# Performance work log

Measured on AMD Instinct MI355X. Metric: run time of the kernel, lower is better.

Reference implementation:

```python
import jax, jax.numpy as jnp
import numpy as np

B, V, NFEAT, INTER, NHID1, NHID12, NCLASS = 131072, 8, 32, 8, 16, 8, 2


def setup_inputs() -> dict:
    key = jax.random.key(0)
    ks = jax.random.split(key, 16)
    # node feature tensor: channel 0 = node type in {0,1}, channels 1..32 = features
    types = jax.random.randint(ks[0], (B, V, 1), 0, 2).astype(jnp.float32)
    feats = jax.random.normal(ks[1], (B, V, NFEAT), dtype=jnp.float32)
    x = jnp.concatenate([types, feats], axis=-1)  # (B, V, 33)
    adj = jax.random.uniform(ks[2], (B, V, V), dtype=jnp.float32)
    edge_attr = jax.random.normal(ks[3], (B, V, V), dtype=jnp.float32)
    s = lambda k, *sh: jax.random.normal(k, sh, dtype=jnp.float32) * 0.1
    return {
        "x": x, "adj": adj, "edge_attr": edge_attr,
        "wa": s(ks[4], INTER, NFEAT), "ba": jnp.zeros((INTER,), jnp.float32),
        "wb": s(ks[5], INTER, NFEAT), "bb": jnp.zeros((INTER,), jnp.float32),
        "w1": s(ks[6], NFEAT, NHID1), "b1": jnp.zeros((NHID1,), jnp.float32),
        "w2": s(ks[7], NHID1, NHID12), "b2": jnp.zeros((NHID12,), jnp.float32),
        "wg": s(ks[8], NHID12, NHID12), "bg": jnp.zeros((NHID12,), jnp.float32),
        "wf": s(ks[9], NCLASS, NHID12), "bf": jnp.zeros((NCLASS,), jnp.float32),
    }


def _attn_pool(h, wg, bg):
    # GlobalAttentionPooling: softmax(gate_nn(h)) over nodes, weighted sum
    gate = jax.nn.softmax(jnp.einsum('bvc,oc->bvo', h, wg) + bg, axis=1)
    return jnp.sum(gate * h, axis=1)  # (B, NHID12)


def reference(x, adj, edge_attr, wa, ba, wb, bb, w1, b1, w2, b2, wg, bg, wf, bf):
    node_types = x[..., 0]           # (B, V)
    feat = x[..., 1:]                # (B, V, 32)
    # conv_b (1x1 conv == per-node linear), output layout (B, inter, V)
    Fk = jnp.einsum('bvc,oc->bov', feat, wb) + bb[None, :, None]  # (B, 8, V=8)
    S = jax.nn.softmax(jnp.matmul(Fk, Fk), axis=1)                # (B, 8, 8)
    W = adj * (S + edge_attr)                                     # (B, V, V)
    # graph conv 1: (W @ feat) @ w1 + b1, LeakyReLU(0.01)
    h = jax.nn.leaky_relu(jnp.einsum('bvw,bwc->bvc', W, feat) @ w1 + b1)
    # graph conv 2
    h = jax.nn.leaky_relu(jnp.einsum('bvw,bwc->bvc', W, h) @ w2 + b2)  # (B, V, 8)
    # per-type masked attention pooling; types fixed to {0, 1}
    pooled = []
    for t in (0.0, 1.0):
        mask = (node_types == t)[..., None].astype(h.dtype)
        pooled.append(_attn_pool(h * mask, wg, bg))
    x_pool = jnp.mean(jnp.stack(pooled, axis=1), axis=1)  # (B, NHID12)
    return x_pool @ wf.T + bf  # (B, NCLASS)
```

## Files before the change

### kernel.cpp

```cpp
#include <hip/hip_runtime.h>


#define SLOTS 32
#define NTHREADS 256

typedef float v2f __attribute__((ext_vector_type(2)));
typedef float4 __attribute__((aligned(4))) f4u;

__device__ __forceinline__ float grp_sum8(float x) {
    x += __shfl_xor(x, 1);
    x += __shfl_xor(x, 2);
    x += __shfl_xor(x, 4);
    return x;
}
__device__ __forceinline__ void wavefence() { __builtin_amdgcn_wave_barrier(); }
__device__ __forceinline__ v2f mkv(float a, float b) { v2f r; r.x = a; r.y = b; return r; }


#define KSTEP(kk, cb) { \
    const float4 qk = *(const float4*)(SB + v * 16 + ((((kk) + (v >> 1) + sl) & 3) << 2)); \
    const v2f fA = mkv(qk.x, qk.y), fB = mkv(qk.z, qk.w); \
    _Pragma("unroll") \
    for (int o = 0; o < 8; ++o) { \
        Fko[o] = __builtin_elementwise_fma(fA, *(const v2f*)(wb + o * 32 + (cb)),     Fko[o]); \
        Fko[o] = __builtin_elementwise_fma(fB, *(const v2f*)(wb + o * 32 + (cb) + 2), Fko[o]); \
    } \
    const float fu[4] = { qk.x, qk.y, qk.z, qk.w }; \
    _Pragma("unroll") \
    for (int u = 0; u < 4; ++u) { \
        const int c = (cb) + u; \
        const v2f f2 = mkv(fu[u], fu[u]); \
        _Pragma("unroll") \
        for (int p = 0; p < 8; ++p) \
            g12[p] = __builtin_elementwise_fma(f2, *(const v2f*)(w1 + c * 16 + 2 * p), g12[p]); \
    } }

__global__ __launch_bounds__(NTHREADS, 4)
void gcn_fused(const float* __restrict__ x,
               const float* __restrict__ adj,
               const float* __restrict__ edge,
               const float* __restrict__ wb, const float* __restrict__ bb,
               const float* __restrict__ w1, const float* __restrict__ b1,
               const float* __restrict__ w2, const float* __restrict__ b2,
               const float* __restrict__ wg,
               const float* __restrict__ wf, const float* __restrict__ bf,
               float* __restrict__ out, int nGroups)
{
    __shared__ __align__(16) float lds[4480];

    const int tid  = threadIdx.x;
    const int slot = tid >> 3;
    const int v    = tid & 7;
    const int sl   = slot & 7;
    float* SB = &lds[(slot >> 3) * 1120 + sl * 140];
    float* A  = SB + 64;

    long long bb_ = (long long)blockIdx.x * SLOTS + slot;
    if (bb_ >= (long long)nGroups * SLOTS) bb_ = (long long)nGroups * SLOTS - 1;
    const size_t b = (size_t)bb_;

    const float* xb = x + b * 264;
    const int nb = v & 4;
    const int cl = v & 3;
    float4 xa[4];
#pragma unroll
    for (int i = 0; i < 4; ++i)
        xa[i] = *(const f4u*)(xb + (nb + i) * 33 + 1 + cl * 4);

    const float4* ar = (const float4*)(adj  + b * 64 + (size_t)v * 8);
    const float4* er = (const float4*)(edge + b * 64 + (size_t)v * 8);
    const float4 a0 = ar[0], a1 = ar[1];
    const float4 e0 = er[0], e1 = er[1];
    const float type = xb[v * 33];

#pragma unroll
    for (int i = 0; i < 4; ++i) {
        const int n = nb + i;
        *(float4*)(SB + n * 16 + (((cl + (n >> 1) + sl) & 3) << 2)) = xa[i];
    }
    float4 xc[4];
#pragma unroll
    for (int i = 0; i < 4; ++i)
        xc[i] = *(const f4u*)(xb + (nb + i) * 33 + 17 + cl * 4);
    wavefence();

    v2f Fko[8];
#pragma unroll
    for (int o = 0; o < 8; ++o) Fko[o] = mkv(0.f, 0.f);
    v2f g12[8];
#pragma unroll
    for (int p = 0; p < 8; ++p) g12[p] = mkv(0.f, 0.f);

    KSTEP(0, 0) KSTEP(1, 4) KSTEP(2, 8) KSTEP(3, 12)
    wavefence();
#pragma unroll
    for (int i = 0; i < 4; ++i) {
        const int n = nb + i;
        *(float4*)(SB + n * 16 + (((cl + (n >> 1) + sl) & 3) << 2)) = xc[i];
    }
    wavefence();
    KSTEP(0, 16) KSTEP(1, 20) KSTEP(2, 24) KSTEP(3, 28)
    wavefence();

    float Fks[8];
#pragma unroll
    for (int o = 0; o < 8; ++o) Fks[o] = Fko[o].x + Fko[o].y + bb[o];

#pragma unroll
    for (int o = 0; o < 8; ++o) A[o * 8 + v] = Fks[o];
    {
        float4* gp = (float4*)(SB + v * 8);
        gp[0] = make_float4(g12[0].x, g12[0].y, g12[1].x, g12[1].y);
        gp[1] = make_float4(g12[2].x, g12[2].y, g12[3].x, g12[3].y);
    }
    wavefence();

    v2f Fk2[4];
#pragma unroll
    for (int p = 0; p < 4; ++p) Fk2[p] = mkv(Fks[2 * p], Fks[2 * p + 1]);

    float M[8];
#pragma unroll
    for (int o = 0; o < 8; ++o) {
        const float4* fr = (const float4*)(A + o * 8);
        const float4 r0 = fr[0], r1 = fr[1];
        v2f acc = mkv(0.f, 0.f);
        acc = __builtin_elementwise_fma(mkv(r0.x, r0.y), Fk2[0], acc);
        acc = __builtin_elementwise_fma(mkv(r0.z, r0.w), Fk2[1], acc);
        acc = __builtin_elementwise_fma(mkv(r1.x, r1.y), Fk2[2], acc);
        acc = __builtin_elementwise_fma(mkv(r1.z, r1.w), Fk2[3], acc);
        M[o] = acc.x + acc.y;
    }
    wavefence();
    float mx = M[0];
#pragma unroll
    for (int o = 1; o < 8; ++o) mx = fmaxf(mx, M[o]);
    float ssum = 0.f;
#pragma unroll
    for (int o = 0; o < 8; ++o) { M[o] = __expf(M[o] - mx); ssum += M[o]; }
    const float sinv = 1.f / ssum;
#pragma unroll
    for (int o = 0; o < 8; ++o) A[o * 8 + v] = M[o] * sinv;
    wavefence();

    const float4* sr = (const float4*)(A + v * 8);
    const float4 s0 = sr[0], s1 = sr[1];
    v2f W2[4];
    W2[0] = mkv(a0.x, a0.y) * (mkv(s0.x, s0.y) + mkv(e0.x, e0.y));
    W2[1] = mkv(a0.z, a0.w) * (mkv(s0.z, s0.w) + mkv(e0.z, e0.w));
    W2[2] = mkv(a1.x, a1.y) * (mkv(s1.x, s1.y) + mkv(e1.x, e1.y));
    W2[3] = mkv(a1.z, a1.w) * (mkv(s1.z, s1.w) + mkv(e1.z, e1.w));

    v2f m1[8];
#pragma unroll
    for (int p = 0; p < 8; ++p) m1[p] = mkv(0.f, 0.f);
#pragma unroll
    for (int w = 0; w < 8; ++w) {
        const float wv = (w & 1) ? W2[w >> 1].y : W2[w >> 1].x;
        const v2f f2 = mkv(wv, wv);
        const float4* gp = (const float4*)(SB + w * 8);
        const float4 q0 = gp[0], q1 = gp[1];
        m1[0] = __builtin_elementwise_fma(f2, mkv(q0.x, q0.y), m1[0]);
        m1[1] = __builtin_elementwise_fma(f2, mkv(q0.z, q0.w), m1[1]);
        m1[2] = __builtin_elementwise_fma(f2, mkv(q1.x, q1.y), m1[2]);
        m1[3] = __builtin_elementwise_fma(f2, mkv(q1.z, q1.w), m1[3]);
    }
    wavefence();
    {
        float4* gp = (float4*)(SB + v * 8);
        gp[0] = make_float4(g12[4].x, g12[4].y, g12[5].x, g12[5].y);
        gp[1] = make_float4(g12[6].x, g12[6].y, g12[7].x, g12[7].y);
    }
    wavefence();
#pragma unroll
    for (int w = 0; w < 8; ++w) {
        const float wv = (w & 1) ? W2[w >> 1].y : W2[w >> 1].x;
        const v2f f2 = mkv(wv, wv);
        const float4* gp = (const float4*)(SB + w * 8);
        const float4 q0 = gp[0], q1 = gp[1];
        m1[4] = __builtin_elementwise_fma(f2, mkv(q0.x, q0.y), m1[4]);
        m1[5] = __builtin_elementwise_fma(f2, mkv(q0.z, q0.w), m1[5]);
        m1[6] = __builtin_elementwise_fma(f2, mkv(q1.x, q1.y), m1[6]);
        m1[7] = __builtin_elementwise_fma(f2, mkv(q1.z, q1.w), m1[7]);
    }
    v2f h[8];
    {
        const v2f k01 = mkv(0.01f, 0.01f);
#pragma unroll
        for (int p = 0; p < 8; ++p) {
            const v2f t = m1[p] + *(const v2f*)(b1 + 2 * p);
            h[p] = __builtin_elementwise_max(t, t * k01);
        }
    }

    v2f g22[4];
#pragma unroll
    for (int p = 0; p < 4; ++p) g22[p] = mkv(0.f, 0.f);
#pragma unroll
    for (int j = 0; j < 16; ++j) {
        const float hv = (j & 1) ? h[j >> 1].y : h[j >> 1].x;
        const v2f f2 = mkv(hv, hv);
#pragma unroll
        for (int p = 0; p < 4; ++p)
            g22[p] = __builtin_elementwise_fma(f2, *(const v2f*)(w2 + j * 8 + 2 * p), g22[p]);
    }
    wavefence();
    {
        float4* gp = (float4*)(SB + v * 8);
        gp[0] = make_float4(g22[0].x, g22[0].y, g22[1].x, g22[1].y);
        gp[1] = make_float4(g22[2].x, g22[2].y, g22[3].x, g22[3].y);
    }
    wavefence();

    v2f m2[4];
#pragma unroll
    for (int p = 0; p < 4; ++p) m2[p] = mkv(0.f, 0.f);
#pragma unroll
    for (int w = 0; w < 8; ++w) {
        const float wv = (w & 1) ? W2[w >> 1].y : W2[w >> 1].x;
        const v2f f2 = mkv(wv, wv);
        const float4* gp = (const float4*)(SB + w * 8);
        const float4 q0 = gp[0], q1 = gp[1];
        m2[0] = __builtin_elementwise_fma(f2, mkv(q0.x, q0.y), m2[0]);
        m2[1] = __builtin_elementwise_fma(f2, mkv(q0.z, q0.w), m2[1]);
        m2[2] = __builtin_elementwise_fma(f2, mkv(q1.x, q1.y), m2[2]);
        m2[3] = __builtin_elementwise_fma(f2, mkv(q1.z, q1.w), m2[3]);
    }
    v2f h2[4];
    {
        const v2f k01 = mkv(0.01f, 0.01f);
#pragma unroll
        for (int p = 0; p < 4; ++p) {
            const v2f t = m2[p] + *(const v2f*)(b2 + 2 * p);
            h2[p] = __builtin_elementwise_max(t, t * k01);
        }
    }

    float Ys[8];
#pragma unroll
    for (int o = 0; o < 8; ++o) {
        v2f acc = mkv(0.f, 0.f);
#pragma unroll
        for (int p = 0; p < 4; ++p)
            acc = __builtin_elementwise_fma(h2[p], *(const v2f*)(wg + o * 8 + 2 * p), acc);
        Ys[o] = acc.x + acc.y;
    }
    wavefence();
    {
        float4* pp = (float4*)(SB + v * 16);
        pp[0] = make_float4(Ys[0], h2[0].x, Ys[1], h2[0].y);
        pp[1] = make_float4(Ys[2], h2[1].x, Ys[3], h2[1].y);
        pp[2] = make_float4(Ys[4], h2[2].x, Ys[5], h2[2].y);
        pp[3] = make_float4(Ys[6], h2[3].x, Ys[7], h2[3].y);
        SB[128 + v] = type;
    }
    wavefence();

    const int o = v;
    float yc[8], hc[8], ty[8];
#pragma unroll
    for (int vp = 0; vp < 8; ++vp) {
        const float2 q = *(const float2*)(SB + vp * 16 + o * 2);
        yc[vp] = q.x;
        hc[vp] = q.y;
        ty[vp] = SB[128 + vp];
    }
    float xp = 0.f;
#pragma unroll
    for (int t = 0; t < 2; ++t) {
        const float tv = (float)t;
        float l[8];
        float lmx = -1e30f;
#pragma unroll
        for (int vp = 0; vp < 8; ++vp) {
            l[vp] = (ty[vp] == tv) ? yc[vp] : 0.f;
            lmx = fmaxf(lmx, l[vp]);
        }
        float esum = 0.f, num = 0.f;
#pragma unroll
        for (int vp = 0; vp < 8; ++vp) {
            const float e = __expf(l[vp] - lmx);
            esum += e;
            num  += (ty[vp] == tv) ? e * hc[vp] : 0.f;
        }
        xp += 0.5f * num / esum;
    }

    const float y0 = grp_sum8(xp * wf[0 * 8 + o]);
    const float y1 = grp_sum8(xp * wf[1 * 8 + o]);
    if (v == 0) {
        float2* op = (float2*)(out + b * 2);
        *op = make_float2(y0 + bf[0], y1 + bf[1]);
    }
}

extern "C" void kernel_launch(void* const* d_in, const int* in_sizes, int n_in,
                              void* d_out, int out_size, void* d_ws, size_t ws_size,
                              hipStream_t stream) {
    const float* x    = (const float*)d_in[0];
    const float* adj  = (const float*)d_in[1];
    const float* edge = (const float*)d_in[2];
    const float* wb   = (const float*)d_in[5];
    const float* bb   = (const float*)d_in[6];
    const float* w1   = (const float*)d_in[7];
    const float* b1   = (const float*)d_in[8];
    const float* w2   = (const float*)d_in[9];
    const float* b2   = (const float*)d_in[10];
    const float* wg   = (const float*)d_in[11];
    const float* wf   = (const float*)d_in[13];
    const float* bf   = (const float*)d_in[14];
    float* out = (float*)d_out;

    const int Btot    = in_sizes[0] / 264;
    const int nGroups = (Btot + SLOTS - 1) / SLOTS;

    gcn_fused<<<nGroups, NTHREADS, 0, stream>>>(x, adj, edge, wb, bb, w1, b1,
                                                w2, b2, wg, wf, bf, out, nGroups);
}
```

Before: 273.2 us.

## Process two graphs per thread group to reuse weight loads and raise ILP

Each 8-thread group now handles two graphs instead of one (64 graphs per block), sharing each weight load across both graphs in the conv, graph-conv and pooling stages. LDS per block doubles, and the adj/edge loads are moved later to overlap with the first feature pass. The aim is to amortise scalar and constant weight loads and expose more independent FMAs per thread. The cost is higher register and LDS pressure, which may reduce occupancy under the 4-blocks launch bound.

New measurement: 283.4 us. 1.04x slower.

```diff
diff --git a/kernel.cpp b/kernel.cpp
--- a/kernel.cpp
+++ b/kernel.cpp
@@ -1,7 +1,7 @@
 #include <hip/hip_runtime.h>
 
 
-#define SLOTS 32
+#define SLOTS 64
 #define NTHREADS 256
 
 typedef float v2f __attribute__((ext_vector_type(2)));
@@ -15,24 +15,37 @@
 }
 __device__ __forceinline__ void wavefence() { __builtin_amdgcn_wave_barrier(); }
 __device__ __forceinline__ v2f mkv(float a, float b) { v2f r; r.x = a; r.y = b; return r; }
-
-
-#define KSTEP(kk, cb) { \
-    const float4 qk = *(const float4*)(SB + v * 16 + ((((kk) + (v >> 1) + sl) & 3) << 2)); \
-    const v2f fA = mkv(qk.x, qk.y), fB = mkv(qk.z, qk.w); \
+__device__ __forceinline__ v2f vfma(v2f a, v2f b, v2f c) { return __builtin_elementwise_fma(a, b, c); }
+
+
+#define KSTEP2(kk, cb) { \
+    const int cell = (((kk) + (v >> 1) + sl) & 3) << 2; \
+    const float4 qA = *(const float4*)(SB0 + v * 16 + cell); \
+    const float4 qB = *(const float4*)(SB1 + v * 16 + cell); \
+    const v2f fA01 = mkv(qA.x, qA.y), fA23 = mkv(qA.z, qA.w); \
+    const v2f fB01 = mkv(qB.x, qB.y), fB23 = mkv(qB.z, qB.w); \
     _Pragma("unroll") \
     for (int o = 0; o < 8; ++o) { \
-        Fko[o] = __builtin_elementwise_fma(fA, *(const v2f*)(wb + o * 32 + (cb)),     Fko[o]); \
-        Fko[o] = __builtin_elementwise_fma(fB, *(const v2f*)(wb + o * 32 + (cb) + 2), Fko[o]); \
+        const v2f w01 = *(const v2f*)(wb + o * 32 + (cb)); \
+        const v2f w23 = *(const v2f*)(wb + o * 32 + (cb) + 2); \
+        Fko[0][o] = vfma(fA01, w01, Fko[0][o]); \
+        Fko[0][o] = vfma(fA23, w23, Fko[0][o]); \
+        Fko[1][o] = vfma(fB01, w01, Fko[1][o]); \
+        Fko[1][o] = vfma(fB23, w23, Fko[1][o]); \
     } \
-    const float fu[4] = { qk.x, qk.y, qk.z, qk.w }; \
+    const float fuA[4] = { qA.x, qA.y, qA.z, qA.w }; \
+    const float fuB[4] = { qB.x, qB.y, qB.z, qB.w }; \
     _Pragma("unroll") \
     for (int u = 0; u < 4; ++u) { \
         const int c = (cb) + u; \
-        const v2f f2 = mkv(fu[u], fu[u]); \
+        const v2f fa = mkv(fuA[u], fuA[u]); \
+        const v2f fb = mkv(fuB[u], fuB[u]); \
         _Pragma("unroll") \
-        for (int p = 0; p < 8; ++p) \
-            g12[p] = __builtin_elementwise_fma(f2, *(const v2f*)(w1 + c * 16 + 2 * p), g12[p]); \
+        for (int p = 0; p < 8; ++p) { \
+            const v2f wp = *(const v2f*)(w1 + c * 16 + 2 * p); \
+            g12[0][p] = vfma(fa, wp, g12[0][p]); \
+            g12[1][p] = vfma(fb, wp, g12[1][p]); \
+        } \
     } }
 
 __global__ __launch_bounds__(NTHREADS, 4)
@@ -46,251 +59,321 @@
                const float* __restrict__ wf, const float* __restrict__ bf,
                float* __restrict__ out, int nGroups)
 {
-    __shared__ __align__(16) float lds[4480];
+    __shared__ __align__(16) float lds[8960];
 
     const int tid  = threadIdx.x;
     const int slot = tid >> 3;
     const int v    = tid & 7;
     const int sl   = slot & 7;
-    float* SB = &lds[(slot >> 3) * 1120 + sl * 140];
-    float* A  = SB + 64;
-
-    long long bb_ = (long long)blockIdx.x * SLOTS + slot;
-    if (bb_ >= (long long)nGroups * SLOTS) bb_ = (long long)nGroups * SLOTS - 1;
-    const size_t b = (size_t)bb_;
-
-    const float* xb = x + b * 264;
+    float* SB0 = &lds[(tid >> 6) * 2240 + sl * 140];
+    float* SB1 = SB0 + 1120;
+    float* SBg[2] = { SB0, SB1 };
+
+    long long base = (long long)blockIdx.x * SLOTS + slot;
+    const long long bmax = (long long)nGroups * SLOTS - 1;
+    size_t b[2];
+#pragma unroll
+    for (int g = 0; g < 2; ++g) {
+        long long t = base + g * 32;
+        if (t > bmax) t = bmax;
+        b[g] = (size_t)t;
+    }
+
+    const float wfv0 = wf[v], wfv1 = wf[8 + v];
+
+    const float* xb[2] = { x + b[0] * 264, x + b[1] * 264 };
     const int nb = v & 4;
     const int cl = v & 3;
-    float4 xa[4];
-#pragma unroll
-    for (int i = 0; i < 4; ++i)
-        xa[i] = *(const f4u*)(xb + (nb + i) * 33 + 1 + cl * 4);
-
-    const float4* ar = (const float4*)(adj  + b * 64 + (size_t)v * 8);
-    const float4* er = (const float4*)(edge + b * 64 + (size_t)v * 8);
-    const float4 a0 = ar[0], a1 = ar[1];
-    const float4 e0 = er[0], e1 = er[1];
-    const float type = xb[v * 33];
-
-#pragma unroll
-    for (int i = 0; i < 4; ++i) {
-        const int n = nb + i;
-        *(float4*)(SB + n * 16 + (((cl + (n >> 1) + sl) & 3) << 2)) = xa[i];
-    }
-    float4 xc[4];
-#pragma unroll
-    for (int i = 0; i < 4; ++i)
-        xc[i] = *(const f4u*)(xb + (nb + i) * 33 + 17 + cl * 4);
-    wavefence();
-
-    v2f Fko[8];
-#pragma unroll
-    for (int o = 0; o < 8; ++o) Fko[o] = mkv(0.f, 0.f);
-    v2f g12[8];
-#pragma unroll
-    for (int p = 0; p < 8; ++p) g12[p] = mkv(0.f, 0.f);
-
-    KSTEP(0, 0) KSTEP(1, 4) KSTEP(2, 8) KSTEP(3, 12)
-    wavefence();
-#pragma unroll
-    for (int i = 0; i < 4; ++i) {
-        const int n = nb + i;
-        *(float4*)(SB + n * 16 + (((cl + (n >> 1) + sl) & 3) << 2)) = xc[i];
-    }
-    wavefence();
-    KSTEP(0, 16) KSTEP(1, 20) KSTEP(2, 24) KSTEP(3, 28)
-    wavefence();
-
-    float Fks[8];
-#pragma unroll
-    for (int o = 0; o < 8; ++o) Fks[o] = Fko[o].x + Fko[o].y + bb[o];
-
-#pragma unroll
-    for (int o = 0; o < 8; ++o) A[o * 8 + v] = Fks[o];
-    {
-        float4* gp = (float4*)(SB + v * 8);
-        gp[0] = make_float4(g12[0].x, g12[0].y, g12[1].x, g12[1].y);
-        gp[1] = make_float4(g12[2].x, g12[2].y, g12[3].x, g12[3].y);
-    }
-    wavefence();
-
-    v2f Fk2[4];
-#pragma unroll
-    for (int p = 0; p < 4; ++p) Fk2[p] = mkv(Fks[2 * p], Fks[2 * p + 1]);
-
-    float M[8];
-#pragma unroll
-    for (int o = 0; o < 8; ++o) {
-        const float4* fr = (const float4*)(A + o * 8);
-        const float4 r0 = fr[0], r1 = fr[1];
-        v2f acc = mkv(0.f, 0.f);
-        acc = __builtin_elementwise_fma(mkv(r0.x, r0.y), Fk2[0], acc);
-        acc = __builtin_elementwise_fma(mkv(r0.z, r0.w), Fk2[1], acc);
-        acc = __builtin_elementwise_fma(mkv(r1.x, r1.y), Fk2[2], acc);
-        acc = __builtin_elementwise_fma(mkv(r1.z, r1.w), Fk2[3], acc);
-        M[o] = acc.x + acc.y;
-    }
-    wavefence();
-    float mx = M[0];
-#pragma unroll
-    for (int o = 1; o < 8; ++o) mx = fmaxf(mx, M[o]);
-    float ssum = 0.f;
-#pragma unroll
-    for (int o = 0; o < 8; ++o) { M[o] = __expf(M[o] - mx); ssum += M[o]; }
-    const float sinv = 1.f / ssum;
-#pragma unroll
-    for (int o = 0; o < 8; ++o) A[o * 8 + v] = M[o] * sinv;
-    wavefence();
-
-    const float4* sr = (const float4*)(A + v * 8);
-    const float4 s0 = sr[0], s1 = sr[1];
-    v2f W2[4];
-    W2[0] = mkv(a0.x, a0.y) * (mkv(s0.x, s0.y) + mkv(e0.x, e0.y));
-    W2[1] = mkv(a0.z, a0.w) * (mkv(s0.z, s0.w) + mkv(e0.z, e0.w));
-    W2[2] = mkv(a1.x, a1.y) * (mkv(s1.x, s1.y) + mkv(e1.x, e1.y));
-    W2[3] = mkv(a1.z, a1.w) * (mkv(s1.z, s1.w) + mkv(e1.z, e1.w));
-
-    v2f m1[8];
-#pragma unroll
-    for (int p = 0; p < 8; ++p) m1[p] = mkv(0.f, 0.f);
-#pragma unroll
-    for (int w = 0; w < 8; ++w) {
-        const float wv = (w & 1) ? W2[w >> 1].y : W2[w >> 1].x;
-        const v2f f2 = mkv(wv, wv);
-        const float4* gp = (const float4*)(SB + w * 8);
-        const float4 q0 = gp[0], q1 = gp[1];
-        m1[0] = __builtin_elementwise_fma(f2, mkv(q0.x, q0.y), m1[0]);
-        m1[1] = __builtin_elementwise_fma(f2, mkv(q0.z, q0.w), m1[1]);
-        m1[2] = __builtin_elementwise_fma(f2, mkv(q1.x, q1.y), m1[2]);
-        m1[3] = __builtin_elementwise_fma(f2, mkv(q1.z, q1.w), m1[3]);
-    }
-    wavefence();
-    {
-        float4* gp = (float4*)(SB + v * 8);
-        gp[0] = make_float4(g12[4].x, g12[4].y, g12[5].x, g12[5].y);
-        gp[1] = make_float4(g12[6].x, g12[6].y, g12[7].x, g12[7].y);
-    }
-    wavefence();
-#pragma unroll
-    for (int w = 0; w < 8; ++w) {
-        const float wv = (w & 1) ? W2[w >> 1].y : W2[w >> 1].x;
-        const v2f f2 = mkv(wv, wv);
-        const float4* gp = (const float4*)(SB + w * 8);
-        const float4 q0 = gp[0], q1 = gp[1];
-        m1[4] = __builtin_elementwise_fma(f2, mkv(q0.x, q0.y), m1[4]);
-        m1[5] = __builtin_elementwise_fma(f2, mkv(q0.z, q0.w), m1[5]);
-        m1[6] = __builtin_elementwise_fma(f2, mkv(q1.x, q1.y), m1[6]);
-        m1[7] = __builtin_elementwise_fma(f2, mkv(q1.z, q1.w), m1[7]);
-    }
-    v2f h[8];
+    float4 xa[2][4];
+#pragma unroll
+    for (int g = 0; g < 2; ++g)
+#pragma unroll
+        for (int i = 0; i < 4; ++i)
+            xa[g][i] = *(const f4u*)(xb[g] + (nb + i) * 33 + 1 + cl * 4);
+
+#pragma unroll
+    for (int g = 0; g < 2; ++g) SBg[g][128 + v] = xb[g][v * 33];
+
+#pragma unroll
+    for (int g = 0; g < 2; ++g)
+#pragma unroll
+        for (int i = 0; i < 4; ++i) {
+            const int n = nb + i;
+            *(float4*)(SBg[g] + n * 16 + (((cl + (n >> 1) + sl) & 3) << 2)) = xa[g][i];
+        }
+    float4 xc[2][4];
+#pragma unroll
+    for (int g = 0; g < 2; ++g)
+#pragma unroll
+        for (int i = 0; i < 4; ++i)
+            xc[g][i] = *(const f4u*)(xb[g] + (nb + i) * 33 + 17 + cl * 4);
+    wavefence();
+
+    v2f Fko[2][8];
+    v2f g12[2][8];
+#pragma unroll
+    for (int g = 0; g < 2; ++g)
+#pragma unroll
+        for (int p = 0; p < 8; ++p) { Fko[g][p] = mkv(0.f, 0.f); g12[g][p] = mkv(0.f, 0.f); }
+
+    KSTEP2(0, 0) KSTEP2(1, 4) KSTEP2(2, 8) KSTEP2(3, 12)
+    wavefence();
+#pragma unroll
+    for (int g = 0; g < 2; ++g)
+#pragma unroll
+        for (int i = 0; i < 4; ++i) {
+            const int n = nb + i;
+            *(float4*)(SBg[g] + n * 16 + (((cl + (n >> 1) + sl) & 3) << 2)) = xc[g][i];
+        }
+    wavefence();
+
+    float4 a0[2], a1[2], e0[2], e1[2];
+#pragma unroll
+    for (int g = 0; g < 2; ++g) {
+        const float4* ar = (const float4*)(adj  + b[g] * 64 + (size_t)v * 8);
+        const float4* er = (const float4*)(edge + b[g] * 64 + (size_t)v * 8);
+        a0[g] = ar[0]; a1[g] = ar[1];
+        e0[g] = er[0]; e1[g] = er[1];
+    }
+
+    KSTEP2(0, 16) KSTEP2(1, 20) KSTEP2(2, 24) KSTEP2(3, 28)
+    wavefence();
+
+    float Fks[2][8];
+#pragma unroll
+    for (int g = 0; g < 2; ++g)
+#pragma unroll
+        for (int o = 0; o < 8; ++o) Fks[g][o] = Fko[g][o].x + Fko[g][o].y + bb[o];
+
+#pragma unroll
+    for (int g = 0; g < 2; ++g) {
+        float* A = SBg[g] + 64;
+#pragma unroll
+        for (int o = 0; o < 8; ++o) A[o * 8 + v] = Fks[g][o];
+        float4* gp = (float4*)(SBg[g] + v * 8);
+        gp[0] = make_float4(g12[g][0].x, g12[g][0].y, g12[g][1].x, g12[g][1].y);
+        gp[1] = make_float4(g12[g][2].x, g12[g][2].y, g12[g][3].x, g12[g][3].y);
+    }
+    wavefence();
+
+    v2f Fk2[2][4];
+#pragma unroll
+    for (int g = 0; g < 2; ++g)
+#pragma unroll
+        for (int p = 0; p < 4; ++p) Fk2[g][p] = mkv(Fks[g][2 * p], Fks[g][2 * p + 1]);
+
+    float M[2][8];
+#pragma unroll
+    for (int g = 0; g < 2; ++g) {
+        const float* A = SBg[g] + 64;
+#pragma unroll
+        for (int o = 0; o < 8; ++o) {
+            const float4* fr = (const float4*)(A + o * 8);
+            const float4 r0 = fr[0], r1 = fr[1];
+            v2f acc = mkv(0.f, 0.f);
+            acc = vfma(mkv(r0.x, r0.y), Fk2[g][0], acc);
+            acc = vfma(mkv(r0.z, r0.w), Fk2[g][1], acc);
+            acc = vfma(mkv(r1.x, r1.y), Fk2[g][2], acc);
+            acc = vfma(mkv(r1.z, r1.w), Fk2[g][3], acc);
+            M[g][o] = acc.x + acc.y;
+        }
+    }
+    wavefence();
+
+#pragma unroll
+    for (int g = 0; g < 2; ++g) {
+        float mx = M[g][0];
+#pragma unroll
+        for (int o = 1; o < 8; ++o) mx = fmaxf(mx, M[g][o]);
+        float ssum = 0.f;
+#pragma unroll
+        for (int o = 0; o < 8; ++o) { M[g][o] = __expf(M[g][o] - mx); ssum += M[g][o]; }
+        const float sinv = 1.f / ssum;
+        float* A = SBg[g] + 64;
+#pragma unroll
+        for (int o = 0; o < 8; ++o) A[o * 8 + v] = M[g][o] * sinv;
+    }
+    wavefence();
+
+    v2f W2[2][4];
+#pragma unroll
+    for (int g = 0; g < 2; ++g) {
+        const float4* sr = (const float4*)(SBg[g] + 64 + v * 8);
+        const float4 s0 = sr[0], s1 = sr[1];
+        W2[g][0] = mkv(a0[g].x, a0[g].y) * (mkv(s0.x, s0.y) + mkv(e0[g].x, e0[g].y));
+        W2[g][1] = mkv(a0[g].z, a0[g].w) * (mkv(s0.z, s0.w) + mkv(e0[g].z, e0[g].w));
+        W2[g][2] = mkv(a1[g].x, a1[g].y) * (mkv(s1.x, s1.y) + mkv(e1[g].x, e1[g].y));
+        W2[g][3] = mkv(a1[g].z, a1[g].w) * (mkv(s1.z, s1.w) + mkv(e1[g].z, e1[g].w));
+    }
+
+    v2f m1[2][8];
+#pragma unroll
+    for (int g = 0; g < 2; ++g)
+#pragma unroll
+        for (int p = 0; p < 8; ++p) m1[g][p] = mkv(0.f, 0.f);
+#pragma unroll
+    for (int g = 0; g < 2; ++g)
+#pragma unroll
+        for (int w = 0; w < 8; ++w) {
+            const float wv = (w & 1) ? W2[g][w >> 1].y : W2[g][w >> 1].x;
+            const v2f f2 = mkv(wv, wv);
+            const float4* gp = (const float4*)(SBg[g] + w * 8);
+            const float4 q0 = gp[0], q1 = gp[1];
+            m1[g][0] = vfma(f2, mkv(q0.x, q0.y), m1[g][0]);
+            m1[g][1] = vfma(f2, mkv(q0.z, q0.w), m1[g][1]);
+            m1[g][2] = vfma(f2, mkv(q1.x, q1.y), m1[g][2]);
+            m1[g][3] = vfma(f2, mkv(q1.z, q1.w), m1[g][3]);
+        }
+    wavefence();
+#pragma unroll
+    for (int g = 0; g < 2; ++g) {
+        float4* gp = (float4*)(SBg[g] + v * 8);
+        gp[0] = make_float4(g12[g][4].x, g12[g][4].y, g12[g][5].x, g12[g][5].y);
+        gp[1] = make_float4(g12[g][6].x, g12[g][6].y, g12[g][7].x, g12[g][7].y);
+    }
+    wavefence();
+#pragma unroll
+    for (int g = 0; g < 2; ++g)
+#pragma unroll
+        for (int w = 0; w < 8; ++w) {
+            const float wv = (w & 1) ? W2[g][w >> 1].y : W2[g][w >> 1].x;
+            const v2f f2 = mkv(wv, wv);
+            const float4* gp = (const float4*)(SBg[g] + w * 8);
+            const float4 q0 = gp[0], q1 = gp[1];
+            m1[g][4] = vfma(f2, mkv(q0.x, q0.y), m1[g][4]);
+            m1[g][5] = vfma(f2, mkv(q0.z, q0.w), m1[g][5]);
+            m1[g][6] = vfma(f2, mkv(q1.x, q1.y), m1[g][6]);
+            m1[g][7] = vfma(f2, mkv(q1.z, q1.w), m1[g][7]);
+        }
+    v2f h[2][8];
     {
         const v2f k01 = mkv(0.01f, 0.01f);
 #pragma unroll
-        for (int p = 0; p < 8; ++p) {
-            const v2f t = m1[p] + *(const v2f*)(b1 + 2 * p);
-            h[p] = __builtin_elementwise_max(t, t * k01);
-        }
-    }
-
-    v2f g22[4];
-#pragma unroll
-    for (int p = 0; p < 4; ++p) g22[p] = mkv(0.f, 0.f);
+        for (int g = 0; g < 2; ++g)
+#pragma unroll
+            for (int p = 0; p < 8; ++p) {
+                const v2f t = m1[g][p] + *(const v2f*)(b1 + 2 * p);
+                h[g][p] = __builtin_elementwise_max(t, t * k01);
+            }
+    }
+
+    v2f g22[2][4];
+#pragma unroll
+    for (int g = 0; g < 2; ++g)
+#pragma unroll
+        for (int p = 0; p < 4; ++p) g22[g][p] = mkv(0.f, 0.f);
 #pragma unroll
     for (int j = 0; j < 16; ++j) {
-        const float hv = (j & 1) ? h[j >> 1].y : h[j >> 1].x;
-        const v2f f2 = mkv(hv, hv);
-#pragma unroll
-        for (int p = 0; p < 4; ++p)
-            g22[p] = __builtin_elementwise_fma(f2, *(const v2f*)(w2 + j * 8 + 2 * p), g22[p]);
-    }
-    wavefence();
-    {
-        float4* gp = (float4*)(SB + v * 8);
-        gp[0] = make_float4(g22[0].x, g22[0].y, g22[1].x, g22[1].y);
-        gp[1] = make_float4(g22[2].x, g22[2].y, g22[3].x, g22[3].y);
-    }
-    wavefence();
-
-    v2f m2[4];
-#pragma unroll
-    for (int p = 0; p < 4; ++p) m2[p] = mkv(0.f, 0.f);
-#pragma unroll
-    for (int w = 0; w < 8; ++w) {
-        const float wv = (w & 1) ? W2[w >> 1].y : W2[w >> 1].x;
-        const v2f f2 = mkv(wv, wv);
-        const float4* gp = (const float4*)(SB + w * 8);
-        const float4 q0 = gp[0], q1 = gp[1];
-        m2[0] = __builtin_elementwise_fma(f2, mkv(q0.x, q0.y), m2[0]);
-        m2[1] = __builtin_elementwise_fma(f2, mkv(q0.z, q0.w), m2[1]);
-        m2[2] = __builtin_elementwise_fma(f2, mkv(q1.x, q1.y), m2[2]);
-        m2[3] = __builtin_elementwise_fma(f2, mkv(q1.z, q1.w), m2[3]);
-    }
-    v2f h2[4];
+        const float hA = (j & 1) ? h[0][j >> 1].y : h[0][j >> 1].x;
+        const float hB = (j & 1) ? h[1][j >> 1].y : h[1][j >> 1].x;
+        const v2f fa = mkv(hA, hA), fb = mkv(hB, hB);
+#pragma unroll
+        for (int p = 0; p < 4; ++p) {
+            const v2f wp = *(const v2f*)(w2 + j * 8 + 2 * p);
+            g22[0][p] = vfma(fa, wp, g22[0][p]);
+            g22[1][p] = vfma(fb, wp, g22[1][p]);
+        }
+    }
+    wavefence();
+#pragma unroll
+    for (int g = 0; g < 2; ++g) {
+        float4* gp = (float4*)(SBg[g] + v * 8);
+        gp[0] = make_float4(g22[g][0].x, g22[g][0].y, g22[g][1].x, g22[g][1].y);
+        gp[1] = make_float4(g22[g][2].x, g22[g][2].y, g22[g][3].x, g22[g][3].y);
+    }
+    wavefence();
+
+    v2f m2[2][4];
+#pragma unroll
+    for (int g = 0; g < 2; ++g)
+#pragma unroll
+        for (int p = 0; p < 4; ++p) m2[g][p] = mkv(0.f, 0.f);
+#pragma unroll
+    for (int g = 0; g < 2; ++g)
+#pragma unroll
+        for (int w = 0; w < 8; ++w) {
+            const float wv = (w & 1) ? W2[g][w >> 1].y : W2[g][w >> 1].x;
+            const v2f f2 = mkv(wv, wv);
+            const float4* gp = (const float4*)(SBg[g] + w * 8);
+            const float4 q0 = gp[0], q1 = gp[1];
+            m2[g][0] = vfma(f2, mkv(q0.x, q0.y), m2[g][0]);
+            m2[g][1] = vfma(f2, mkv(q0.z, q0.w), m2[g][1]);
+            m2[g][2] = vfma(f2, mkv(q1.x, q1.y), m2[g][2]);
+            m2[g][3] = vfma(f2, mkv(q1.z, q1.w), m2[g][3]);
+        }
+    v2f h2[2][4];
     {
         const v2f k01 = mkv(0.01f, 0.01f);
 #pragma unroll
+        for (int g = 0; g < 2; ++g)
+#pragma unroll
+            for (int p = 0; p < 4; ++p) {
+                const v2f t = m2[g][p] + *(const v2f*)(b2 + 2 * p);
+                h2[g][p] = __builtin_elementwise_max(t, t * k01);
+            }
+    }
+
+    float Ys[2][8];
+#pragma unroll
+    for (int o = 0; o < 8; ++o) {
+        v2f aA = mkv(0.f, 0.f), aB = mkv(0.f, 0.f);
+#pragma unroll
         for (int p = 0; p < 4; ++p) {
-            const v2f t = m2[p] + *(const v2f*)(b2 + 2 * p);
-            h2[p] = __builtin_elementwise_max(t, t * k01);
-        }
-    }
-
-    float Ys[8];
-#pragma unroll
-    for (int o = 0; o < 8; ++o) {
-        v2f acc = mkv(0.f, 0.f);
-#pragma unroll
-        for (int p = 0; p < 4; ++p)
-            acc = __builtin_elementwise_fma(h2[p], *(const v2f*)(wg + o * 8 + 2 * p), acc);
-        Ys[o] = acc.x + acc.y;
-    }
-    wavefence();
-    {
-        float4* pp = (float4*)(SB + v * 16);
-        pp[0] = make_float4(Ys[0], h2[0].x, Ys[1], h2[0].y);
-        pp[1] = make_float4(Ys[2], h2[1].x, Ys[3], h2[1].y);
-        pp[2] = make_float4(Ys[4], h2[2].x, Ys[5], h2[2].y);
-        pp[3] = make_float4(Ys[6], h2[3].x, Ys[7], h2[3].y);
-        SB[128 + v] = type;
+            const v2f wp = *(const v2f*)(wg + o * 8 + 2 * p);
+            aA = vfma(h2[0][p], wp, aA);
+            aB = vfma(h2[1][p], wp, aB);
+        }
+        Ys[0][o] = aA.x + aA.y;
+        Ys[1][o] = aB.x + aB.y;
+    }
+    wavefence();
+#pragma unroll
+    for (int g = 0; g < 2; ++g) {
+        float4* pp = (float4*)(SBg[g] + v * 16);
+        pp[0] = make_float4(Ys[g][0], h2[g][0].x, Ys[g][1], h2[g][0].y);
+        pp[1] = make_float4(Ys[g][2], h2[g][1].x, Ys[g][3], h2[g][1].y);
+        pp[2] = make_float4(Ys[g][4], h2[g][2].x, Ys[g][5], h2[g][2].y);
+        pp[3] = make_float4(Ys[g][6], h2[g][3].x, Ys[g][7], h2[g][3].y);
     }
     wavefence();
 
     const int o = v;
-    float yc[8], hc[8], ty[8];
-#pragma unroll
-    for (int vp = 0; vp < 8; ++vp) {
-        const float2 q = *(const float2*)(SB + vp * 16 + o * 2);
-        yc[vp] = q.x;
-        hc[vp] = q.y;
-        ty[vp] = SB[128 + vp];
-    }
-    float xp = 0.f;
-#pragma unroll
-    for (int t = 0; t < 2; ++t) {
-        const float tv = (float)t;
-        float l[8];
-        float lmx = -1e30f;
+#pragma unroll
+    for (int g = 0; g < 2; ++g) {
+        float yc[8], hc[8], ty[8];
 #pragma unroll
         for (int vp = 0; vp < 8; ++vp) {
-            l[vp] = (ty[vp] == tv) ? yc[vp] : 0.f;
-            lmx = fmaxf(lmx, l[vp]);
-        }
-        float esum = 0.f, num = 0.f;
-#pragma unroll
-        for (int vp = 0; vp < 8; ++vp) {
-            const float e = __expf(l[vp] - lmx);
-            esum += e;
-            num  += (ty[vp] == tv) ? e * hc[vp] : 0.f;
-        }
-        xp += 0.5f * num / esum;
-    }
-
-    const float y0 = grp_sum8(xp * wf[0 * 8 + o]);
-    const float y1 = grp_sum8(xp * wf[1 * 8 + o]);
-    if (v == 0) {
-        float2* op = (float2*)(out + b * 2);
-        *op = make_float2(y0 + bf[0], y1 + bf[1]);
+            const float2 q = *(const float2*)(SBg[g] + vp * 16 + o * 2);
+            yc[vp] = q.x;
+            hc[vp] = q.y;
+            ty[vp] = SBg[g][128 + vp];
+        }
+        float xp = 0.f;
+#pragma unroll
+        for (int t = 0; t < 2; ++t) {
+            const float tv = (float)t;
+            float l[8];
+            float lmx = -1e30f;
+#pragma unroll
+            for (int vp = 0; vp < 8; ++vp) {
+                l[vp] = (ty[vp] == tv) ? yc[vp] : 0.f;
+                lmx = fmaxf(lmx, l[vp]);
+            }
+            float esum = 0.f, num = 0.f;
+#pragma unroll
+            for (int vp = 0; vp < 8; ++vp) {
+                const float e = __expf(l[vp] - lmx);
+                esum += e;
+                num  += (ty[vp] == tv) ? e * hc[vp] : 0.f;
+            }
+            xp += 0.5f * num / esum;
+        }
+        const float y0 = grp_sum8(xp * wfv0);
+        const float y1 = grp_sum8(xp * wfv1);
+        if (v == 0) {
+            float2* op = (float2*)(out + b[g] * 2);
+            *op = make_float2(y0 + bf[0], y1 + bf[1]);
+        }
     }
 }
 
```
